# Performance work log

Hardware: AMD Instinct MI355X
Metric: run time of the kernel (lower is better)

## Reference

```python
import jax, jax.numpy as jnp
import numpy as np
from jax import lax

LONG_EDGE = 1024
MAX_SIZE = 1333.0
STRIDES = (4, 8, 16, 32, 64)
SIZES = (32, 64, 128, 256, 512)
RATIOS = (0.5, 1.0, 2.0)
PRE_NMS_TOPK = 6000
POST_NMS_TOPK = 1000
NMS_THRESH = 0.7
NUM_CH = 256


def _gen_anchors_level(scale, ratios, shape, stride):
    # faithful copy of generate_anchors_keras (numpy, static)
    scales, ratios = np.meshgrid(np.array([scale], dtype=np.float64), np.array(ratios, dtype=np.float64))
    scales = scales.flatten(); ratios = ratios.flatten()
    size_ratios = stride * stride / ratios
    widths = np.round(np.sqrt(size_ratios))
    heights = np.round(widths * ratios)
    widths = widths * (scales / stride)
    heights = heights * (scales / stride)
    shifts_y = np.arange(0, shape[0]) * stride + (stride - 1) / 2
    shifts_x = np.arange(0, shape[1]) * stride + (stride - 1) / 2
    shifts_x, shifts_y = np.meshgrid(shifts_x, shifts_y)
    box_widths, box_centers_x = np.meshgrid(widths, shifts_x)
    box_heights, box_centers_y = np.meshgrid(heights, shifts_y)
    box_centers = np.stack([box_centers_y, box_centers_x], axis=2).reshape([-1, 2])
    box_sizes = np.stack([box_heights, box_widths], axis=2).reshape([-1, 2])
    boxes = np.concatenate([box_centers - 0.5 * (box_sizes - 1), box_centers + 0.5 * (box_sizes - 1)], axis=1)
    boxes[:, [2, 3]] += 1
    return boxes[:, [1, 0, 3, 2]].astype(np.float32)


def all_anchors():
    shapes = [(int(np.ceil(LONG_EDGE / s)),) * 2 for s in STRIDES]
    return np.concatenate([_gen_anchors_level(SIZES[i], RATIOS, shapes[i], STRIDES[i]) for i in range(len(STRIDES))], axis=0)


def conv2d(x, w, b, padding):
    y = lax.conv_general_dilated(x, w, (1, 1), padding, dimension_numbers=('NCHW', 'OIHW', 'NCHW'))
    return y + b[None, :, None, None]


def decode_bbox_target(deltas, anchors):
    # deltas, anchors: [K,4]
    txty, twth = deltas[:, :2], deltas[:, 2:]
    x1y1, x2y2 = anchors[:, :2], anchors[:, 2:]
    waha = x2y2 - x1y1
    xaya = (x2y2 + x1y1) * 0.5
    clipv = jnp.float32(np.log(MAX_SIZE / 16.0))
    wbhb = jnp.exp(jnp.minimum(twth, clipv)) * waha
    xbyb = txty * waha + xaya
    return jnp.concatenate([xbyb - wbhb * 0.5, xbyb + wbhb * 0.5], axis=1)


def clip_boxes(b, h, w):
    # faithful to source: x clamped to window[0]=h, y to window[1]=w
    return jnp.stack([b[:, 0].clip(0.0, h), b[:, 1].clip(0.0, w), b[:, 2].clip(0.0, h), b[:, 3].clip(0.0, w)], 1)


def nms_keep(boxes, thresh):
    # boxes sorted by descending score; greedy NMS over full IoU matrix
    x1, y1, x2, y2 = boxes[:, 0], boxes[:, 1], boxes[:, 2], boxes[:, 3]
    areas = (x2 - x1) * (y2 - y1)
    iw = jnp.clip(jnp.minimum(x2[:, None], x2[None, :]) - jnp.maximum(x1[:, None], x1[None, :]), 0.0)
    ih = jnp.clip(jnp.minimum(y2[:, None], y2[None, :]) - jnp.maximum(y1[:, None], y1[None, :]), 0.0)
    inter = iw * ih
    iou = inter / (areas[:, None] + areas[None, :] - inter)
    n = boxes.shape[0]
    sup = iou > thresh
    idxs = jnp.arange(n)
    def body(i, keep):
        row = sup[i] & (idxs > i)
        return jnp.where(keep[i], keep & ~row, keep)
    return lax.fori_loop(0, n, body, jnp.ones((n,), bool))


def rpn_forward(image, feats, w0, b0, wcls, bcls, wbox, bbox):
    labels, boxes_l = [], []
    for f in feats:
        hidden = jax.nn.relu(conv2d(f, w0, b0, 'SAME'))
        cls = conv2d(hidden, wcls, bcls, 'VALID')   # [1,A,H,W]
        box = conv2d(hidden, wbox, bbox, 'VALID')   # [1,4A,H,W]
        labels.append(jnp.transpose(cls, (0, 2, 3, 1)).reshape(1, -1, 1))
        boxes_l.append(jnp.transpose(box, (0, 2, 3, 1)).reshape(1, -1, 4))
    scores = jnp.concatenate(labels, axis=1)[0, :, 0]          # [N]
    box_logits = jnp.concatenate(boxes_l, axis=1)[0]           # [N,4]
    anchors = jnp.asarray(all_anchors())                       # [N,4]
    k = min(PRE_NMS_TOPK, anchors.shape[0])
    _, order = lax.top_k(scores, k)
    deltas = box_logits[order]
    pre_anch = anchors[order]
    dec = decode_bbox_target(deltas, pre_anch)
    h, w = float(image.shape[2]), float(image.shape[3])
    boxes = clip_boxes(dec, h, w)
    keep = nms_keep(lax.stop_gradient(boxes), NMS_THRESH)
    sel = jnp.argsort(~keep)[:POST_NMS_TOPK]  # stable: kept boxes in score order, then pad slots
    proposals = jnp.where(keep[sel][:, None], boxes[sel], 0.0)
    return proposals


def setup_inputs() -> dict:
    key = jax.random.key(0)
    ks = jax.random.split(key, 9)
    hw = [256, 128, 64, 32, 16]
    inp = {'image': jax.random.normal(ks[0], (1, 3, 1024, 1024), jnp.float32)}
    for i, s in enumerate(hw):
        inp[f'feat{i}'] = jax.random.normal(jax.random.fold_in(ks[1], i), (1, NUM_CH, s, s), jnp.float32)
    inp['w0'] = jax.random.normal(ks[2], (NUM_CH, NUM_CH, 3, 3), jnp.float32) * 0.01
    inp['b0'] = jnp.zeros((NUM_CH,), jnp.float32)
    inp['wcls'] = jax.random.normal(ks[3], (3, NUM_CH, 1, 1), jnp.float32) * 0.01
    inp['bcls'] = jnp.zeros((3,), jnp.float32)
    inp['wbox'] = jax.random.normal(ks[4], (12, NUM_CH, 1, 1), jnp.float32) * 0.01
    inp['bbox'] = jnp.zeros((12,), jnp.float32)
    return inp


def reference(image, feat0, feat1, feat2, feat3, feat4, w0, b0, wcls, bcls, wbox, bbox):
    feats = [feat0, feat1, feat2, feat3, feat4]
    return rpn_forward(image, feats, w0, b0, wcls, bcls, wbox, bbox)
```

## Files before the change

### kernel.cpp

```cpp
#include <hip/hip_runtime.h>
#include <cstdint>

typedef unsigned long long u64;
typedef unsigned int u32;
typedef unsigned short ushort;
typedef __attribute__((ext_vector_type(8))) short short8;
typedef __attribute__((ext_vector_type(4))) float f32x4;
typedef __attribute__((ext_vector_type(4))) double f64x4;

#define A_TOTAL 261888
#define NPIX    87296
#define KTOP    6000
#define KTARGET 7800
#define NWORDS  94
#define CANDMAX 8192
#define PIXMAX  8192
#define NBINS   16384

#if defined(__has_builtin)
#if __has_builtin(__builtin_amdgcn_mfma_f64_16x16x4f64)
#define HAVE_DGEMM 1
#endif
#endif
#ifndef HAVE_DGEMM
#define HAVE_DGEMM 0
#endif

__device__ __forceinline__ u64 score_key64(double s) {
  u64 u = (u64)__double_as_longlong(s);
  return (u & 0x8000000000000000ULL) ? ~u : (u | 0x8000000000000000ULL);
}
__device__ __forceinline__ u32 key32(float s) {
  u32 u = __float_as_uint(s);
  return (u & 0x80000000u) ? ~u : (u | 0x80000000u);
}
__device__ __forceinline__ ushort f2bf(float f) {
  u32 u = __float_as_uint(f);
  u32 r = (u + 0x7FFFu + ((u >> 16) & 1u)) >> 16;
  return (ushort)r;
}
__device__ __forceinline__ void pix_level(int pix, int& l, int& off) {
  if (pix < 65536)      { l = 0; off = 0; }
  else if (pix < 81920) { l = 1; off = 65536; }
  else if (pix < 86016) { l = 2; off = 81920; }
  else if (pix < 87040) { l = 3; off = 86016; }
  else                  { l = 4; off = 87040; }
}

__global__ void k_prep_w(const float* __restrict__ w0, double* __restrict__ wt64,
                         ushort* __restrict__ wkf) {
  int i = blockIdx.x * 256 + threadIdx.x;
  if (i < 256 * 2304) {
    int o = i & 255;
    int ictap = i >> 8;
    float v = w0[o * 2304 + ictap];
    wt64[(size_t)ictap * 256 + o] = (double)v;
    int ic = ictap / 9;
    int tap = ictap - ic * 9;
    int w = o >> 6, mt = (o >> 4) & 3, l15 = o & 15;
    int ch = ic >> 5, kk = ic & 31;
    int l4 = kk >> 3, e = kk & 7;
    int lane = l4 * 16 + l15;
    wkf[((((w * 4 + mt) * 8 + ch) * 9 + tap) << 9) + lane * 8 + e] = f2bf(v);
  }
}

__global__ void k_probe(u32* __restrict__ flag) {
#if HAVE_DGEMM
  int l = threadIdx.x;
  int m = l & 15, kq = l >> 4;
  double a = (double)(1 + m * 4 + kq);
  double b = (double)(1 + m * 4 + kq * 67);
  f64x4 c = {0.0, 0.0, 0.0, 0.0};
  c = __builtin_amdgcn_mfma_f64_16x16x4f64(a, b, c, 0, 0, 0);
  bool ok = true;
  #pragma unroll
  for (int r = 0; r < 4; ++r) {
    int row = 4 * kq + r, col = m;
    double e = 0.0;
    for (int k = 0; k < 4; ++k)
      e += (double)(1 + row * 4 + k) * (double)(1 + col * 4 + k * 67);
    if (c[r] != e) ok = false;
  }
  u64 bal = __ballot(ok);
  if (l == 0) *flag = (bal == ~0ULL) ? 1u : 0u;
#else
  if (threadIdx.x == 0) *flag = 0u;
#endif
}

__global__ __launch_bounds__(256, 2) void k_conv_mfma(
    const float* __restrict__ f0, const float* __restrict__ f1,
    const float* __restrict__ f2, const float* __restrict__ f3,
    const float* __restrict__ f4,
    const ushort* __restrict__ wkf, const float* __restrict__ b0,
    const float* __restrict__ wcls, const float* __restrict__ bcls,
    float* __restrict__ scr)
{
  __shared__ ushort xsl[100][40];
  __shared__ float  part[3][64][17];

  int b = blockIdx.x;
  int l, tb;
  if (b < 1024)      { l = 0; tb = b; }
  else if (b < 1280) { l = 1; tb = b - 1024; }
  else if (b < 1344) { l = 2; tb = b - 1280; }
  else if (b < 1360) { l = 3; tb = b - 1344; }
  else               { l = 4; tb = b - 1360; }
  const float* feat = (l == 0) ? f0 : (l == 1) ? f1 : (l == 2) ? f2 : (l == 3) ? f3 : f4;
  int Hh = 256 >> l;
  int HW = Hh * Hh;
  int pixOff = (l == 0) ? 0 : (l == 1) ? 65536 : (l == 2) ? 81920 : (l == 3) ? 86016 : 87040;
  int shl = 5 - l;
  int ty = (tb >> shl) << 3;
  int tx = (tb & ((1 << shl) - 1)) << 3;

  int tid = threadIdx.x;
  int w = tid >> 6;
  int lane = tid & 63;
  int l15 = lane & 15;
  int l4 = lane >> 4;

  f32x4 zz = {0.f, 0.f, 0.f, 0.f};
  f32x4 acc[4][4];
  #pragma unroll
  for (int mt = 0; mt < 4; ++mt)
    #pragma unroll
    for (int tt = 0; tt < 4; ++tt) acc[mt][tt] = zz;

  for (int ch = 0; ch < 8; ++ch) {
    __syncthreads();
    for (int e = tid; e < 3200; e += 256) {
      int icl = e / 100;
      int sp = e - icl * 100;
      int yy = sp / 10;
      int xx = sp - yy * 10;
      int gy = ty + yy - 1, gx = tx + xx - 1;
      float v = 0.f;
      if (gy >= 0 && gy < Hh && gx >= 0 && gx < Hh)
        v = feat[(ch * 32 + icl) * HW + gy * Hh + gx];
      xsl[sp][icl] = f2bf(v);
    }
    __syncthreads();
    #pragma unroll
    for (int tap = 0; tap < 9; ++tap) {
      int dy = tap / 3;
      int dx = tap - dy * 3;
      short8 af[4], bf[4];
      #pragma unroll
      for (int mt = 0; mt < 4; ++mt) {
        int abase = ((((w * 4 + mt) * 8 + ch) * 9 + tap) << 9) + (lane << 3);
        af[mt] = *(const short8*)(wkf + abase);
      }
      #pragma unroll
      for (int tt = 0; tt < 4; ++tt) {
        int p = (tt << 4) + l15;
        int sp = ((p >> 3) + dy) * 10 + (p & 7) + dx;
        bf[tt] = *(const short8*)&xsl[sp][l4 << 3];
      }
      #pragma unroll
      for (int mt = 0; mt < 4; ++mt)
        #pragma unroll
        for (int tt = 0; tt < 4; ++tt)
          acc[mt][tt] = __builtin_amdgcn_mfma_f32_16x16x32_bf16(af[mt], bf[tt], acc[mt][tt], 0, 0, 0);
    }
  }

  float pr[3][4];
  #pragma unroll
  for (int kk = 0; kk < 3; ++kk)
    #pragma unroll
    for (int tt = 0; tt < 4; ++tt) pr[kk][tt] = 0.f;
  #pragma unroll
  for (int mt = 0; mt < 4; ++mt) {
    #pragma unroll
    for (int r = 0; r < 4; ++r) {
      int oc = (w << 6) + (mt << 4) + (l4 << 2) + r;
      float bb = b0[oc];
      float c0 = wcls[oc], c1 = wcls[256 + oc], c2 = wcls[512 + oc];
      #pragma unroll
      for (int tt = 0; tt < 4; ++tt) {
        float v = acc[mt][tt][r] + bb;
        v = v > 0.f ? v : 0.f;
        pr[0][tt] = fmaf(c0, v, pr[0][tt]);
        pr[1][tt] = fmaf(c1, v, pr[1][tt]);
        pr[2][tt] = fmaf(c2, v, pr[2][tt]);
      }
    }
  }
  __syncthreads();
  #pragma unroll
  for (int kk = 0; kk < 3; ++kk)
    #pragma unroll
    for (int tt = 0; tt < 4; ++tt)
      part[kk][(tt << 4) + l15][(w << 2) + l4] = pr[kk][tt];
  __syncthreads();
  if (tid < 192) {
    int kk = tid >> 6;
    int px = tid & 63;
    float s = 0.f;
    #pragma unroll
    for (int q = 0; q < 16; ++q) s += part[kk][px][q];
    int pix = pixOff + (ty + (px >> 3)) * Hh + (tx + (px & 7));
    scr[pix * 3 + kk] = s + bcls[kk];
  }
}

__global__ void k_hist1(const float* __restrict__ scr, u32* __restrict__ bins) {
  __shared__ u32 h[NBINS];
  int tid = threadIdx.x;
  for (int idx = tid; idx < NBINS; idx += 256) h[idx] = 0;
  __syncthreads();
  for (int i = blockIdx.x * 256 + tid; i < A_TOTAL; i += gridDim.x * 256)
    atomicAdd(&h[key32(scr[i]) >> 18], 1u);
  __syncthreads();
  for (int idx = tid; idx < NBINS; idx += 256) {
    u32 v = h[idx];
    if (v) atomicAdd(&bins[idx], v);
  }
}

__global__ void k_scan1(const u32* __restrict__ bins, u32* __restrict__ meta) {
  __shared__ u32 psum[256];
  int tid = threadIdx.x;
  u32 s = 0;
  for (int u = 0; u < 64; ++u) s += bins[tid * 64 + u];
  psum[tid] = s;
  __syncthreads();
  if (tid == 0) {
    u32 run = 0;
    for (int t = 255; t >= 0; --t) { u32 tmp = psum[t]; psum[t] = run; run += tmp; }
  }
  __syncthreads();
  u32 cum = psum[tid];
  if (cum < (u32)KTARGET) {
    for (int u = 63; u >= 0; --u) {
      u32 bv = bins[tid * 64 + u];
      u32 nc = cum + bv;
      if (nc >= (u32)KTARGET) {
        meta[0] = (u32)(tid * 64 + u);
        meta[2] = cum;
        break;
      }
      cum = nc;
    }
  }
}

__global__ void k_hist2(const float* __restrict__ scr, const u32* __restrict__ meta,
                        u32* __restrict__ sub) {
  int i = blockIdx.x * 256 + threadIdx.x;
  if (i < A_TOTAL) {
    u32 k = key32(scr[i]);
    if ((k >> 18) == meta[0]) atomicAdd(&sub[(k >> 10) & 0xFFu], 1u);
  }
}

__global__ void k_scan2(const u32* __restrict__ sub, u32* __restrict__ meta) {
  if (threadIdx.x == 0) {
    u32 b = meta[0];
    u32 c = meta[2];
    u32 T = b << 18;
    for (int u = 255; u >= 0; --u) {
      c += sub[u];
      if (c >= (u32)KTARGET) { T = (b << 18) | ((u32)u << 10); break; }
    }
    meta[3] = (T >= (2u << 10)) ? (T - (2u << 10)) : 0u;
  }
}

__global__ void k_cnt2(const float* __restrict__ scr, const u32* __restrict__ meta,
                       u32* __restrict__ blkCnt, u32* __restrict__ blkCntP) {
  __shared__ u32 wc[4], wcp[4];
  int tid = threadIdx.x;
  int lane = tid & 63, wv = tid >> 6;
  u32 T = meta[3];
  int i = blockIdx.x * 256 + tid;
  bool qa = (i < A_TOTAL) && (key32(scr[i]) >= T);
  u64 ba = __ballot(qa);
  bool qp = false;
  if (i < NPIX)
    qp = (key32(scr[i * 3 + 0]) >= T) || (key32(scr[i * 3 + 1]) >= T) || (key32(scr[i * 3 + 2]) >= T);
  u64 bp = __ballot(qp);
  if (lane == 0) { wc[wv] = (u32)__popcll(ba); wcp[wv] = (u32)__popcll(bp); }
  __syncthreads();
  if (tid == 0) {
    blkCnt[blockIdx.x]  = wc[0] + wc[1] + wc[2] + wc[3];
    blkCntP[blockIdx.x] = wcp[0] + wcp[1] + wcp[2] + wcp[3];
  }
}

__global__ __launch_bounds__(1024) void k_scanblk2(const u32* __restrict__ blkCnt,
                                                   u32* __restrict__ blkOff,
                                                   u32* __restrict__ totA,
                                                   const u32* __restrict__ blkCntP,
                                                   u32* __restrict__ blkOffP,
                                                   u32* __restrict__ totP) {
  __shared__ u32 buf[2][1024];
  int tid = threadIdx.x;
  for (int pass = 0; pass < 2; ++pass) {
    const u32* src_ = pass ? blkCntP : blkCnt;
    u32* dst_ = pass ? blkOffP : blkOff;
    u32* tot_ = pass ? totP : totA;
    u32 v = (tid < 1023) ? src_[tid] : 0u;
    buf[0][tid] = v;
    __syncthreads();
    int src = 0;
    for (int d = 1; d < 1024; d <<= 1) {
      u32 t = buf[src][tid] + ((tid >= d) ? buf[src][tid - d] : 0u);
      buf[src ^ 1][tid] = t;
      src ^= 1;
      __syncthreads();
    }
    if (tid < 1023) dst_[tid] = buf[src][tid] - v;
    if (tid == 0) tot_[0] = buf[src][1022];
    __syncthreads();
  }
}

__global__ void k_fill2(const float* __restrict__ scr, const u32* __restrict__ meta,
                        const u32* __restrict__ blkOff, const u32* __restrict__ blkOffP,
                        u32* __restrict__ candIdx, u32* __restrict__ pixList,
                        u32* __restrict__ pixMap) {
  __shared__ u32 wbase[4], wbaseP[4];
  int tid = threadIdx.x;
  int lane = tid & 63, wv = tid >> 6;
  u32 T = meta[3];
  int i = blockIdx.x * 256 + tid;
  bool qa = (i < A_TOTAL) && (key32(scr[i]) >= T);
  u64 ba = __ballot(qa);
  bool qp = false;
  if (i < NPIX)
    qp = (key32(scr[i * 3 + 0]) >= T) || (key32(scr[i * 3 + 1]) >= T) || (key32(scr[i * 3 + 2]) >= T);
  u64 bp = __ballot(qp);
  if (lane == 0) { wbase[wv] = (u32)__popcll(ba); wbaseP[wv] = (u32)__popcll(bp); }
  __syncthreads();
  if (tid == 0) {
    u32 r = blkOff[blockIdx.x];
    #pragma unroll
    for (int w2 = 0; w2 < 4; ++w2) { u32 t = wbase[w2]; wbase[w2] = r; r += t; }
    u32 rp = blkOffP[blockIdx.x];
    #pragma unroll
    for (int w2 = 0; w2 < 4; ++w2) { u32 t = wbaseP[w2]; wbaseP[w2] = rp; rp += t; }
  }
  __syncthreads();
  if (qa) {
    u32 rank = (u32)__popcll(ba & ((1ULL << lane) - 1ULL));
    u32 pos = wbase[wv] + rank;
    if (pos < CANDMAX) candIdx[pos] = (u32)i;
  }
  if (qp) {
    u32 rank = (u32)__popcll(bp & ((1ULL << lane) - 1ULL));
    u32 pos = wbaseP[wv] + rank;
    if (pos < PIXMAX) { pixList[pos] = (u32)i; pixMap[i] = pos; }
  }
}

#define KCH 288
__global__ __launch_bounds__(256, 3) void k_hidden_mfma(
    const float* __restrict__ f0, const float* __restrict__ f1,
    const float* __restrict__ f2, const float* __restrict__ f3,
    const float* __restrict__ f4,
    const double* __restrict__ wt64, const float* __restrict__ b0,
    const u32* __restrict__ pixList, const u32* __restrict__ meta,
    double* __restrict__ hbuf)
{
#if HAVE_DGEMM
  __shared__ float patch[2][KCH][16];
  __shared__ int sValid[16], sY[16], sX[16], sW[16], sL[16];
  if (meta[8] == 0) return;
  int tid = threadIdx.x;
  int base = blockIdx.x * 16;
  u32 np = meta[4];
  if (np > PIXMAX) np = PIXMAX;
  if (base >= (int)np) return;

  if (tid < 16) {
    int slot = base + tid;
    int v = slot < (int)np;
    sValid[tid] = v;
    int pix = v ? (int)pixList[slot] : 0;
    int l, off;
    pix_level(pix, l, off);
    int W = 256 >> l;
    int idx = pix - off;
    sL[tid] = l;
    sW[tid] = W;
    sY[tid] = idx >> (8 - l);
    sX[tid] = idx & (W - 1);
  }
  __syncthreads();

  auto stage = [&](int cb, int pb) {
    for (int t = tid; t < 1536; t += 256) {
      int s = t & 15;
      int rem = t >> 4;
      int icl = rem / 3;
      int dy = rem - icl * 3;
      int ic = cb * 32 + icl;
      float v0 = 0.f, v1 = 0.f, v2 = 0.f;
      if (sValid[s]) {
        int l = sL[s], W = sW[s], y = sY[s], x = sX[s];
        const float* feat = (l == 0) ? f0 : (l == 1) ? f1 : (l == 2) ? f2 : (l == 3) ? f3 : f4;
        int gy = y + dy - 1;
        if (gy >= 0 && gy < W) {
          const float* rowp = feat + ic * W * W + gy * W;
          if (x - 1 >= 0) v0 = rowp[x - 1];
          v1 = rowp[x];
          if (x + 1 < W) v2 = rowp[x + 1];
        }
      }
      int kb = icl * 9 + dy * 3;
      patch[pb][kb + 0][s] = v0;
      patch[pb][kb + 1][s] = v1;
      patch[pb][kb + 2][s] = v2;
    }
  };

  int lane = tid & 63, w = tid >> 6;
  int m = lane & 15, kq = lane >> 4;
  f64x4 acc[4];
  #pragma unroll
  for (int mt = 0; mt < 4; ++mt) acc[mt] = f64x4{0.0, 0.0, 0.0, 0.0};

  stage(0, 0);
  __syncthreads();
  for (int cb = 0; cb < 8; ++cb) {
    if (cb < 7) stage(cb + 1, (cb + 1) & 1);
    const float (*pc)[16] = patch[cb & 1];
    for (int ks = 0; ks < KCH / 4; ++ks) {
      double bv = (double)pc[ks * 4 + kq][m];
      const double* wr = wt64 + (size_t)(cb * KCH + ks * 4 + kq) * 256 + w * 64 + m;
      #pragma unroll
      for (int mt = 0; mt < 4; ++mt)
        acc[mt] = __builtin_amdgcn_mfma_f64_16x16x4f64(wr[mt * 16], bv, acc[mt], 0, 0, 0);
    }
    __syncthreads();
  }

  int slot = base + m;
  bool pv = sValid[m];
  #pragma unroll
  for (int mt = 0; mt < 4; ++mt) {
    #pragma unroll
    for (int r = 0; r < 4; ++r) {
      int oc = w * 64 + mt * 16 + 4 * kq + r;
      if (pv) {
        double t2 = acc[mt][r] + (double)b0[oc];
        hbuf[(size_t)slot * 256 + oc] = t2 > 0.0 ? t2 : 0.0;
      }
    }
  }
#endif
}

#define KC 576
__global__ __launch_bounds__(256, 4) void k_hidden_valu(
    const float* __restrict__ f0, const float* __restrict__ f1,
    const float* __restrict__ f2, const float* __restrict__ f3,
    const float* __restrict__ f4,
    const double* __restrict__ wt64, const float* __restrict__ b0,
    const u32* __restrict__ pixList, const u32* __restrict__ meta,
    double* __restrict__ hbuf)
{
  __shared__ __align__(16) float patch[2][KC][8];
  __shared__ int sValid[8], sY[8], sX[8], sW[8], sL[8];
  if (meta[8] != 0) return;

  int tid = threadIdx.x;
  int base = blockIdx.x * 8;
  u32 np = meta[4];
  if (np > PIXMAX) np = PIXMAX;
  if (base >= (int)np) return;

  if (tid < 8) {
    int slot = base + tid;
    int v = slot < (int)np;
    sValid[tid] = v;
    int pix = v ? (int)pixList[slot] : 0;
    int l, off;
    pix_level(pix, l, off);
    int W = 256 >> l;
    int idx = pix - off;
    sL[tid] = l;
    sW[tid] = W;
    sY[tid] = idx >> (8 - l);
    sX[tid] = idx & (W - 1);
  }
  __syncthreads();

  auto stage = [&](int c, int pb) {
    for (int t = tid; t < 1536; t += 256) {
      int s = t / 192;
      int rem = t - s * 192;
      int icl = rem / 3;
      int dy = rem - icl * 3;
      int ic = c * 64 + icl;
      float v0 = 0.f, v1 = 0.f, v2 = 0.f;
      if (sValid[s]) {
        int l = sL[s], W = sW[s], y = sY[s], x = sX[s];
        const float* feat = (l == 0) ? f0 : (l == 1) ? f1 : (l == 2) ? f2 : (l == 3) ? f3 : f4;
        int gy = y + dy - 1;
        if (gy >= 0 && gy < W) {
          const float* rowp = feat + ic * W * W + gy * W;
          if (x - 1 >= 0) v0 = rowp[x - 1];
          v1 = rowp[x];
          if (x + 1 < W) v2 = rowp[x + 1];
        }
      }
      int kb = icl * 9 + dy * 3;
      patch[pb][kb + 0][s] = v0;
      patch[pb][kb + 1][s] = v1;
      patch[pb][kb + 2][s] = v2;
    }
  };

  stage(0, 0);
  __syncthreads();

  double h[8];
  #pragma unroll
  for (int s = 0; s < 8; ++s) h[s] = 0.0;

  for (int c = 0; c < 4; ++c) {
    if (c < 3) stage(c + 1, (c + 1) & 1);
    const double* wcol = wt64 + (size_t)(c * KC) * 256 + tid;
    const float (*pc)[8] = patch[c & 1];
    for (int kk = 0; kk < KC; ++kk) {
      double wv_ = wcol[(size_t)kk * 256];
      float4 pa = *(const float4*)&pc[kk][0];
      float4 pb2 = *(const float4*)&pc[kk][4];
      h[0] = fma(wv_, (double)pa.x, h[0]);
      h[1] = fma(wv_, (double)pa.y, h[1]);
      h[2] = fma(wv_, (double)pa.z, h[2]);
      h[3] = fma(wv_, (double)pa.w, h[3]);
      h[4] = fma(wv_, (double)pb2.x, h[4]);
      h[5] = fma(wv_, (double)pb2.y, h[5]);
      h[6] = fma(wv_, (double)pb2.z, h[6]);
      h[7] = fma(wv_, (double)pb2.w, h[7]);
    }
    __syncthreads();
  }

  double bb = (double)b0[tid];
  #pragma unroll
  for (int s = 0; s < 8; ++s) {
    if (sValid[s]) {
      double t = h[s] + bb;
      hbuf[(size_t)(base + s) * 256 + tid] = t > 0.0 ? t : 0.0;
    }
  }
}

__global__ __launch_bounds__(256, 4) void k_heads(
    const float* __restrict__ wcls, const float* __restrict__ bcls,
    const float* __restrict__ wbox, const float* __restrict__ bbox,
    const u32* __restrict__ candIdx, const u32* __restrict__ pixMap,
    const u32* __restrict__ meta, const double* __restrict__ hbuf,
    u64* __restrict__ candKey, u32* __restrict__ candPack, double* __restrict__ candDelta)
{
  __shared__ double wavePart[8][5][4];
  __shared__ int sIdx[8], sValid[8], sR[8], sPS[8];
  int tid = threadIdx.x;
  int lane = tid & 63;
  int wv = tid >> 6;
  int base = blockIdx.x * 8;
  u32 cnt = meta[1];
  if (cnt > CANDMAX) cnt = CANDMAX;

  if (base >= (int)cnt) {
    if (tid < 8) {
      candKey[base + tid] = 0ULL;
      candPack[base + tid] = 0xFFFFFFFFu;
    }
    return;
  }

  if (tid < 8) {
    int slot = base + tid;
    int v = slot < (int)cnt;
    sValid[tid] = v;
    int aidx = v ? (int)candIdx[slot] : 0;
    sIdx[tid] = aidx;
    int pix = aidx / 3;
    sR[tid] = aidx - pix * 3;
    sPS[tid] = v ? (int)pixMap[pix] : 0;
  }
  __syncthreads();

  for (int s = 0; s < 8; ++s) {
    if (!sValid[s]) continue;
    int r = sR[s];
    double hv = hbuf[(size_t)sPS[s] * 256 + tid];
    double p0 = (double)wcls[r * 256 + tid] * hv;
    double p1 = (double)wbox[(r * 4 + 0) * 256 + tid] * hv;
    double p2 = (double)wbox[(r * 4 + 1) * 256 + tid] * hv;
    double p3 = (double)wbox[(r * 4 + 2) * 256 + tid] * hv;
    double p4 = (double)wbox[(r * 4 + 3) * 256 + tid] * hv;
    #pragma unroll
    for (int d = 32; d; d >>= 1) {
      p0 += __shfl_xor(p0, d);
      p1 += __shfl_xor(p1, d);
      p2 += __shfl_xor(p2, d);
      p3 += __shfl_xor(p3, d);
      p4 += __shfl_xor(p4, d);
    }
    if (lane == 0) {
      wavePart[s][0][wv] = p0;
      wavePart[s][1][wv] = p1;
      wavePart[s][2][wv] = p2;
      wavePart[s][3][wv] = p3;
      wavePart[s][4][wv] = p4;
    }
  }
  __syncthreads();
  if (tid < 40) {
    int s = tid / 5;
    int k = tid - s * 5;
    int slot = base + s;
    if (sValid[s]) {
      double v = wavePart[s][k][0] + wavePart[s][k][1] + wavePart[s][k][2] + wavePart[s][k][3];
      int r = sR[s];
      if (k == 0) {
        double sc_ = v + (double)bcls[r];
        candKey[slot] = score_key64(sc_);
        candPack[slot] = ((u32)sIdx[s] << 13) | (u32)slot;
      } else {
        candDelta[(size_t)slot * 4 + (k - 1)] = v + (double)bbox[r * 4 + (k - 1)];
      }
    } else if (k == 0) {
      candKey[slot] = 0ULL;
      candPack[slot] = 0xFFFFFFFFu;
    }
  }
}

__global__ __launch_bounds__(256) void k_rank(const u64* __restrict__ candKey,
                                              const u32* __restrict__ candPack,
                                              u32* __restrict__ order) {
  __shared__ u64 fk[1024];
  __shared__ u32 fp[1024];
  __shared__ u32 rsum[32][8];
  int tid = threadIdx.x;
  int c = tid & 31;
  int g = tid >> 5;
  int ci = blockIdx.x * 32 + c;
  u64 mk = candKey[ci];
  u32 mp = candPack[ci];
  u32 cnt = 0;
  for (int chunk = 0; chunk < 8; ++chunk) {
    __syncthreads();
    for (int e = tid; e < 1024; e += 256) {
      fk[e] = candKey[chunk * 1024 + e];
      fp[e] = candPack[chunk * 1024 + e];
    }
    __syncthreads();
    int j0 = g * 128;
    #pragma unroll 4
    for (int j = j0; j < j0 + 128; ++j) {
      u64 kj = fk[j];
      cnt += (kj > mk || (kj == mk && fp[j] < mp)) ? 1u : 0u;
    }
  }
  rsum[c][g] = cnt;
  __syncthreads();
  if (tid < 32) {
    u32 rank = 0;
    #pragma unroll
    for (int q = 0; q < 8; ++q) rank += rsum[tid][q];
    if (rank < (u32)KTOP) order[rank] = mp;
  }
}

__global__ void k_decode(const u32* __restrict__ order, const double* __restrict__ candDelta,
                         double* __restrict__ boxesD) {
  int i = blockIdx.x * 64 + threadIdx.x;
  if (i >= KTOP) return;
  u32 pack = order[i];
  u32 slot = pack & 0x1FFFu;
  u32 a = pack >> 13;
  int pix = (int)(a / 3u);
  int r = (int)(a - (u32)pix * 3u);
  int l, off;
  pix_level(pix, l, off);
  int W = 256 >> l;
  int idx = pix - off;
  int y = idx >> (8 - l);
  int x = idx & (W - 1);
  int s = 4 << l;
  double ratio = (r == 0) ? 0.5 : (r == 1) ? 1.0 : 2.0;
  double wq = rint(sqrt((double)(s * s) / ratio));
  double hq = rint(wq * ratio);
  double Wa = wq * 8.0, Ha = hq * 8.0;
  double cx = (double)x * (double)s + (double)(s - 1) * 0.5;
  double cy = (double)y * (double)s + (double)(s - 1) * 0.5;
  double ax1 = (double)(float)(cx - 0.5 * (Wa - 1.0));
  double ay1 = (double)(float)(cy - 0.5 * (Ha - 1.0));
  double ax2 = (double)(float)(cx + 0.5 * (Wa - 1.0) + 1.0);
  double ay2 = (double)(float)(cy + 0.5 * (Ha - 1.0) + 1.0);
  double tx = candDelta[(size_t)slot * 4 + 0], tyv = candDelta[(size_t)slot * 4 + 1];
  double tw = candDelta[(size_t)slot * 4 + 2], th  = candDelta[(size_t)slot * 4 + 3];
  double wa = ax2 - ax1, ha = ay2 - ay1;
  double xa = (ax1 + ax2) * 0.5, ya = (ay1 + ay2) * 0.5;
  double clipv = (double)(float)log(1333.0 / 16.0);
  double wb = exp(fmin(tw, clipv)) * wa;
  double hb = exp(fmin(th, clipv)) * ha;
  double xb = tx * wa + xa;
  double yb = tyv * ha + ya;
  double bx1 = xb - 0.5 * wb, by1 = yb - 0.5 * hb;
  double bx2 = xb + 0.5 * wb, by2 = yb + 0.5 * hb;
  bx1 = fmin(fmax(bx1, 0.0), 1024.0);
  by1 = fmin(fmax(by1, 0.0), 1024.0);
  bx2 = fmin(fmax(bx2, 0.0), 1024.0);
  by2 = fmin(fmax(by2, 0.0), 1024.0);
  boxesD[(size_t)i * 4 + 0] = bx1;
  boxesD[(size_t)i * 4 + 1] = by1;
  boxesD[(size_t)i * 4 + 2] = bx2;
  boxesD[(size_t)i * 4 + 3] = by2;
}

__global__ void k_mask(const double* __restrict__ boxesD, u64* __restrict__ maskA) {
  __shared__ double cbx[64][4];
  int lane = threadIdx.x;
  int bc = blockIdx.x, br = blockIdx.y;
  if (bc < br) return;
  int ci = bc * 64 + lane;
  if (ci < KTOP) {
    cbx[lane][0] = boxesD[(size_t)ci * 4 + 0];
    cbx[lane][1] = boxesD[(size_t)ci * 4 + 1];
    cbx[lane][2] = boxesD[(size_t)ci * 4 + 2];
    cbx[lane][3] = boxesD[(size_t)ci * 4 + 3];
  } else {
    cbx[lane][0] = -1e30; cbx[lane][1] = -1e30; cbx[lane][2] = -1e30; cbx[lane][3] = -1e30;
  }
  __syncthreads();
  int ri = br * 64 + lane;
  if (ri >= KTOP) return;
  double rx1 = boxesD[(size_t)ri * 4 + 0], ry1 = boxesD[(size_t)ri * 4 + 1];
  double rx2 = boxesD[(size_t)ri * 4 + 2], ry2 = boxesD[(size_t)ri * 4 + 3];
  double ra = (rx2 - rx1) * (ry2 - ry1);
  u64 bits = 0;
  #pragma unroll 4
  for (int j = 0; j < 64; ++j) {
    int cj = bc * 64 + j;
    double iw = fmin(rx2, cbx[j][2]) - fmax(rx1, cbx[j][0]);
    double ih = fmin(ry2, cbx[j][3]) - fmax(ry1, cbx[j][1]);
    iw = fmax(iw, 0.0); ih = fmax(ih, 0.0);
    double inter = iw * ih;
    double ca = (cbx[j][2] - cbx[j][0]) * (cbx[j][3] - cbx[j][1]);
    double iou = inter / (ra + ca - inter);
    if (cj > ri && iou > 0.7) bits |= (1ULL << j);
  }
  maskA[(size_t)ri * NWORDS + bc] = bits;
}

__global__ __launch_bounds__(1024) void k_nms_reduce(const u64* __restrict__ maskA,
                                                     u32* __restrict__ keep) {
  __shared__ u64 rm[NWORDS];
  int tid = threadIdx.x;
  int wv = tid >> 6, lane = tid & 63;
  for (int i = tid; i < NWORDS; i += 1024) rm[i] = 0ULL;
  __syncthreads();
  u64 diagNext = maskA[(size_t)lane * NWORDS + 0];
  int keptTot = 0;
  for (int c = 0; c < NWORDS; ++c) {
    int rows = KTOP - c * 64; if (rows > 64) rows = 64;
    u64 validM = (rows == 64) ? ~0ULL : ((1ULL << rows) - 1ULL);
    size_t rowbase = (size_t)(c * 64 + lane) * NWORDS;
    bool lv = lane < rows;
    int w0i = c + wv;
    u64 v0 = (lv && w0i      < NWORDS) ? maskA[rowbase + w0i]      : 0ULL;
    u64 v1 = (lv && w0i + 16 < NWORDS) ? maskA[rowbase + w0i + 16] : 0ULL;
    u64 v2 = (lv && w0i + 32 < NWORDS) ? maskA[rowbase + w0i + 32] : 0ULL;
    u64 v3 = (lv && w0i + 48 < NWORDS) ? maskA[rowbase + w0i + 48] : 0ULL;
    u64 v4 = (lv && w0i + 64 < NWORDS) ? maskA[rowbase + w0i + 64] : 0ULL;
    u64 v5 = (lv && w0i + 80 < NWORDS) ? maskA[rowbase + w0i + 80] : 0ULL;
    u64 diag = diagNext;
    if (c + 1 < NWORDS) {
      int nrows = KTOP - (c + 1) * 64; if (nrows > 64) nrows = 64;
      diagNext = (lane < nrows) ? maskA[(size_t)((c + 1) * 64 + lane) * NWORDS + (c + 1)] : 0ULL;
    }
    u64 R = rm[c];
    u64 undec = (~R) & validM;
    u64 km = 0;
    while (undec) {
      int j = __builtin_ctzll(undec);
      km |= (1ULL << j);
      u64 dj = (u64)__shfl((unsigned long long)diag, j);
      undec &= ~(dj | (1ULL << j));
    }
    if (wv == 0 && lane < rows) keep[c * 64 + lane] = (u32)((km >> lane) & 1ULL);
    keptTot += (int)__popcll(km);
    if (keptTot >= 1000) {
      for (int i = (c + 1) * 64 + tid; i < KTOP; i += 1024) keep[i] = 0u;
      return;
    }
    u64 sel = ((km >> lane) & 1ULL) ? ~0ULL : 0ULL;
    v0 &= sel; v1 &= sel; v2 &= sel; v3 &= sel; v4 &= sel; v5 &= sel;
    #pragma unroll
    for (int s = 32; s; s >>= 1) {
      v0 |= (u64)__shfl_xor((unsigned long long)v0, s);
      v1 |= (u64)__shfl_xor((unsigned long long)v1, s);
      v2 |= (u64)__shfl_xor((unsigned long long)v2, s);
      v3 |= (u64)__shfl_xor((unsigned long long)v3, s);
      v4 |= (u64)__shfl_xor((unsigned long long)v4, s);
      v5 |= (u64)__shfl_xor((unsigned long long)v5, s);
    }
    if (lane == 0) {
      if (w0i      < NWORDS) rm[w0i]      |= v0;
      if (w0i + 16 < NWORDS) rm[w0i + 16] |= v1;
      if (w0i + 32 < NWORDS) rm[w0i + 32] |= v2;
      if (w0i + 48 < NWORDS) rm[w0i + 48] |= v3;
      if (w0i + 64 < NWORDS) rm[w0i + 64] |= v4;
      if (w0i + 80 < NWORDS) rm[w0i + 80] |= v5;
    }
    __syncthreads();
  }
}

__global__ __launch_bounds__(1024) void k_emit(const u32* __restrict__ keep,
                                               const double* __restrict__ boxesD,
                                               float* __restrict__ out) {
  __shared__ u32 partial[1024];
  __shared__ u32 excl[1024];
  int tid = threadIdx.x;
  for (int j = tid; j < 4000; j += 1024) out[j] = 0.f;
  int base = tid * 6;
  u32 kv[6];
  u32 c = 0;
  #pragma unroll
  for (int u = 0; u < 6; ++u) {
    int j = base + u;
    kv[u] = (j < KTOP) ? keep[j] : 0u;
    c += kv[u];
  }
  partial[tid] = c;
  __syncthreads();
  if (tid == 0) {
    u32 run = 0;
    for (int t = 0; t < 1024; ++t) { excl[t] = run; run += partial[t]; }
  }
  __syncthreads();
  u32 p = excl[tid];
  #pragma unroll
  for (int u = 0; u < 6; ++u) {
    int j = base + u;
    if (j < KTOP && kv[u]) {
      if (p < 1000u) {
        out[p * 4 + 0] = (float)boxesD[(size_t)j * 4 + 0];
        out[p * 4 + 1] = (float)boxesD[(size_t)j * 4 + 1];
        out[p * 4 + 2] = (float)boxesD[(size_t)j * 4 + 2];
        out[p * 4 + 3] = (float)boxesD[(size_t)j * 4 + 3];
      }
      ++p;
    }
  }
}

extern "C" void kernel_launch(void* const* d_in, const int* in_sizes, int n_in,
                              void* d_out, int out_size, void* d_ws, size_t ws_size,
                              hipStream_t stream) {
  const float* f0   = (const float*)d_in[1];
  const float* f1   = (const float*)d_in[2];
  const float* f2   = (const float*)d_in[3];
  const float* f3   = (const float*)d_in[4];
  const float* f4   = (const float*)d_in[5];
  const float* w0   = (const float*)d_in[6];
  const float* b0   = (const float*)d_in[7];
  const float* wcls = (const float*)d_in[8];
  const float* bcls = (const float*)d_in[9];
  const float* wbox = (const float*)d_in[10];
  const float* bbox = (const float*)d_in[11];
  float* out = (float*)d_out;
  char* ws = (char*)d_ws;

  size_t off = 0;
  auto alloc = [&](size_t bytes) { size_t o = off; off += (bytes + 255) & ~(size_t)255; return o; };
  size_t off_scr  = alloc((size_t)A_TOTAL * 4);
  size_t off_w64  = alloc((size_t)256 * 2304 * 8);
  size_t off_wk   = alloc((size_t)256 * 2304 * 2);
  size_t off_hb   = alloc((size_t)PIXMAX * 256 * 8);
  size_t off_ci   = alloc((size_t)CANDMAX * 4);
  size_t off_ck   = alloc((size_t)CANDMAX * 8);
  size_t off_cp   = alloc((size_t)CANDMAX * 4);
  size_t off_cd   = alloc((size_t)CANDMAX * 4 * 8);
  size_t off_pl   = alloc((size_t)PIXMAX * 4);
  size_t off_pm   = alloc((size_t)NPIX * 4);
  size_t off_box  = alloc((size_t)KTOP * 4 * 8);
  size_t off_ord  = alloc((size_t)KTOP * 4);
  size_t off_keep = alloc((size_t)KTOP * 4);
  size_t off_mask = alloc((size_t)KTOP * NWORDS * 8);
  size_t off_bcnt = alloc((size_t)1024 * 4);
  size_t off_boff = alloc((size_t)1024 * 4);
  size_t off_bcp  = alloc((size_t)1024 * 4);
  size_t off_bop  = alloc((size_t)1024 * 4);
  size_t off_bins = alloc((size_t)NBINS * 4);
  size_t off_sub  = alloc((size_t)256 * 4);
  size_t off_meta = alloc((size_t)64 * 4);
  size_t off_end  = off;
  (void)in_sizes; (void)n_in; (void)out_size; (void)ws_size;

  float*  scr       = (float*)(ws + off_scr);
  double* wt64      = (double*)(ws + off_w64);
  ushort* wkf       = (ushort*)(ws + off_wk);
  double* hbuf      = (double*)(ws + off_hb);
  u32*    candIdx   = (u32*)(ws + off_ci);
  u64*    candKey   = (u64*)(ws + off_ck);
  u32*    candPack  = (u32*)(ws + off_cp);
  double* candDelta = (double*)(ws + off_cd);
  u32*    pixList   = (u32*)(ws + off_pl);
  u32*    pixMap    = (u32*)(ws + off_pm);
  double* boxesD    = (double*)(ws + off_box);
  u32*    order     = (u32*)(ws + off_ord);
  u32*    keep      = (u32*)(ws + off_keep);
  u64*    maskA     = (u64*)(ws + off_mask);
  u32*    blkCnt    = (u32*)(ws + off_bcnt);
  u32*    blkOff    = (u32*)(ws + off_boff);
  u32*    blkCntP   = (u32*)(ws + off_bcp);
  u32*    blkOffP   = (u32*)(ws + off_bop);
  u32*    bins      = (u32*)(ws + off_bins);
  u32*    sub       = (u32*)(ws + off_sub);
  u32*    meta      = (u32*)(ws + off_meta);

  hipMemsetAsync(ws + off_bins, 0, off_end - off_bins, stream);

  k_prep_w<<<2304, 256, 0, stream>>>(w0, wt64, wkf);
  k_probe<<<1, 64, 0, stream>>>(meta + 8);
  k_conv_mfma<<<1364, 256, 0, stream>>>(f0, f1, f2, f3, f4, wkf, b0, wcls, bcls, scr);
  k_hist1<<<64, 256, 0, stream>>>(scr, bins);
  k_scan1<<<1, 256, 0, stream>>>(bins, meta);
  k_hist2<<<1023, 256, 0, stream>>>(scr, meta, sub);
  k_scan2<<<1, 64, 0, stream>>>(sub, meta);
  k_cnt2<<<1023, 256, 0, stream>>>(scr, meta, blkCnt, blkCntP);
  k_scanblk2<<<1, 1024, 0, stream>>>(blkCnt, blkOff, meta + 1, blkCntP, blkOffP, meta + 4);
  k_fill2<<<1023, 256, 0, stream>>>(scr, meta, blkOff, blkOffP, candIdx, pixList, pixMap);
  k_hidden_mfma<<<PIXMAX / 16, 256, 0, stream>>>(f0, f1, f2, f3, f4, wt64, b0, pixList, meta, hbuf);
  k_hidden_valu<<<PIXMAX / 8, 256, 0, stream>>>(f0, f1, f2, f3, f4, wt64, b0, pixList, meta, hbuf);
  k_heads<<<CANDMAX / 8, 256, 0, stream>>>(wcls, bcls, wbox, bbox, candIdx, pixMap, meta, hbuf,
                                           candKey, candPack, candDelta);
  k_rank<<<CANDMAX / 32, 256, 0, stream>>>(candKey, candPack, order);
  k_decode<<<94, 64, 0, stream>>>(order, candDelta, boxesD);
  k_mask<<<dim3(NWORDS, NWORDS), 64, 0, stream>>>(boxesD, maskA);
  k_nms_reduce<<<1, 1024, 0, stream>>>(maskA, keep);
  k_emit<<<1, 1024, 0, stream>>>(keep, boxesD, out);
}
```

Measured before the change: 983.7 us.

## Replace FP64 MFMA hidden-layer path with register-tiled FP64 VALU kernel

Removes the runtime DGEMM probe kernel and the dual MFMA/VALU hidden-layer kernels, replacing them with a single kernel. Each thread computes a 4x4 block of output channels by pixels in FP64 FMAs, reading four weights and a float4 of patch values per k-step. On MI355X, where FP64 MFMA is available, this moves the recomputation of hidden activations from matrix cores to vector ALUs. It saves one launch and the probe, but may be slower if FP64 matrix throughput exceeds VALU throughput on this part.

```diff
diff --git a/kernel.cpp b/kernel.cpp
--- a/kernel.cpp
+++ b/kernel.cpp
@@ -6,7 +6,6 @@
 typedef unsigned short ushort;
 typedef __attribute__((ext_vector_type(8))) short short8;
 typedef __attribute__((ext_vector_type(4))) float f32x4;
-typedef __attribute__((ext_vector_type(4))) double f64x4;
 
 #define A_TOTAL 261888
 #define NPIX    87296
@@ -16,15 +15,6 @@
 #define CANDMAX 8192
 #define PIXMAX  8192
 #define NBINS   16384
-
-#if defined(__has_builtin)
-#if __has_builtin(__builtin_amdgcn_mfma_f64_16x16x4f64)
-#define HAVE_DGEMM 1
-#endif
-#endif
-#ifndef HAVE_DGEMM
-#define HAVE_DGEMM 0
-#endif
 
 __device__ __forceinline__ u64 score_key64(double s) {
   u64 u = (u64)__double_as_longlong(s);
@@ -63,30 +53,6 @@
     int lane = l4 * 16 + l15;
     wkf[((((w * 4 + mt) * 8 + ch) * 9 + tap) << 9) + lane * 8 + e] = f2bf(v);
   }
-}
-
-__global__ void k_probe(u32* __restrict__ flag) {
-#if HAVE_DGEMM
-  int l = threadIdx.x;
-  int m = l & 15, kq = l >> 4;
-  double a = (double)(1 + m * 4 + kq);
-  double b = (double)(1 + m * 4 + kq * 67);
-  f64x4 c = {0.0, 0.0, 0.0, 0.0};
-  c = __builtin_amdgcn_mfma_f64_16x16x4f64(a, b, c, 0, 0, 0);
-  bool ok = true;
-  #pragma unroll
-  for (int r = 0; r < 4; ++r) {
-    int row = 4 * kq + r, col = m;
-    double e = 0.0;
-    for (int k = 0; k < 4; ++k)
-      e += (double)(1 + row * 4 + k) * (double)(1 + col * 4 + k * 67);
-    if (c[r] != e) ok = false;
-  }
-  u64 bal = __ballot(ok);
-  if (l == 0) *flag = (bal == ~0ULL) ? 1u : 0u;
-#else
-  if (threadIdx.x == 0) *flag = 0u;
-#endif
 }
 
 __global__ __launch_bounds__(256, 2) void k_conv_mfma(
@@ -357,7 +323,7 @@
 }
 
 #define KCH 288
-__global__ __launch_bounds__(256, 3) void k_hidden_mfma(
+__global__ __launch_bounds__(256, 4) void k_hidden(
     const float* __restrict__ f0, const float* __restrict__ f1,
     const float* __restrict__ f2, const float* __restrict__ f3,
     const float* __restrict__ f4,
@@ -365,10 +331,9 @@
     const u32* __restrict__ pixList, const u32* __restrict__ meta,
     double* __restrict__ hbuf)
 {
-#if HAVE_DGEMM
   __shared__ float patch[2][KCH][16];
   __shared__ int sValid[16], sY[16], sX[16], sW[16], sL[16];
-  if (meta[8] == 0) return;
+
   int tid = threadIdx.x;
   int base = blockIdx.x * 16;
   u32 np = meta[4];
@@ -417,137 +382,61 @@
     }
   };
 
-  int lane = tid & 63, w = tid >> 6;
-  int m = lane & 15, kq = lane >> 4;
-  f64x4 acc[4];
+  int ocq = tid & 63;
+  int pxq = tid >> 6;
+
+  double acc[4][4];
   #pragma unroll
-  for (int mt = 0; mt < 4; ++mt) acc[mt] = f64x4{0.0, 0.0, 0.0, 0.0};
+  for (int i = 0; i < 4; ++i)
+    #pragma unroll
+    for (int j = 0; j < 4; ++j) acc[i][j] = 0.0;
 
   stage(0, 0);
   __syncthreads();
+
   for (int cb = 0; cb < 8; ++cb) {
     if (cb < 7) stage(cb + 1, (cb + 1) & 1);
     const float (*pc)[16] = patch[cb & 1];
-    for (int ks = 0; ks < KCH / 4; ++ks) {
-      double bv = (double)pc[ks * 4 + kq][m];
-      const double* wr = wt64 + (size_t)(cb * KCH + ks * 4 + kq) * 256 + w * 64 + m;
-      #pragma unroll
-      for (int mt = 0; mt < 4; ++mt)
-        acc[mt] = __builtin_amdgcn_mfma_f64_16x16x4f64(wr[mt * 16], bv, acc[mt], 0, 0, 0);
+    const double* wb_ = wt64 + (size_t)(cb * KCH) * 256 + (ocq << 2);
+    for (int kk = 0; kk < KCH; ++kk) {
+      float4 p4 = *(const float4*)&pc[kk][pxq << 2];
+      double pd0 = (double)p4.x, pd1 = (double)p4.y;
+      double pd2 = (double)p4.z, pd3 = (double)p4.w;
+      const double* wr = wb_ + (size_t)kk * 256;
+      double w0_ = wr[0], w1_ = wr[1], w2_ = wr[2], w3_ = wr[3];
+      acc[0][0] = fma(w0_, pd0, acc[0][0]);
+      acc[0][1] = fma(w0_, pd1, acc[0][1]);
+      acc[0][2] = fma(w0_, pd2, acc[0][2]);
+      acc[0][3] = fma(w0_, pd3, acc[0][3]);
+      acc[1][0] = fma(w1_, pd0, acc[1][0]);
+      acc[1][1] = fma(w1_, pd1, acc[1][1]);
+      acc[1][2] = fma(w1_, pd2, acc[1][2]);
+      acc[1][3] = fma(w1_, pd3, acc[1][3]);
+      acc[2][0] = fma(w2_, pd0, acc[2][0]);
+      acc[2][1] = fma(w2_, pd1, acc[2][1]);
+      acc[2][2] = fma(w2_, pd2, acc[2][2]);
+      acc[2][3] = fma(w2_, pd3, acc[2][3]);
+      acc[3][0] = fma(w3_, pd0, acc[3][0]);
+      acc[3][1] = fma(w3_, pd1, acc[3][1]);
+      acc[3][2] = fma(w3_, pd2, acc[3][2]);
+      acc[3][3] = fma(w3_, pd3, acc[3][3]);
     }
     __syncthreads();
   }
 
-  int slot = base + m;
-  bool pv = sValid[m];
+  double bb0 = (double)b0[(ocq << 2) + 0];
+  double bb1 = (double)b0[(ocq << 2) + 1];
+  double bb2 = (double)b0[(ocq << 2) + 2];
+  double bb3 = (double)b0[(ocq << 2) + 3];
   #pragma unroll
-  for (int mt = 0; mt < 4; ++mt) {
-    #pragma unroll
-    for (int r = 0; r < 4; ++r) {
-      int oc = w * 64 + mt * 16 + 4 * kq + r;
-      if (pv) {
-        double t2 = acc[mt][r] + (double)b0[oc];
-        hbuf[(size_t)slot * 256 + oc] = t2 > 0.0 ? t2 : 0.0;
-      }
-    }
-  }
-#endif
-}
-
-#define KC 576
-__global__ __launch_bounds__(256, 4) void k_hidden_valu(
-    const float* __restrict__ f0, const float* __restrict__ f1,
-    const float* __restrict__ f2, const float* __restrict__ f3,
-    const float* __restrict__ f4,
-    const double* __restrict__ wt64, const float* __restrict__ b0,
-    const u32* __restrict__ pixList, const u32* __restrict__ meta,
-    double* __restrict__ hbuf)
-{
-  __shared__ __align__(16) float patch[2][KC][8];
-  __shared__ int sValid[8], sY[8], sX[8], sW[8], sL[8];
-  if (meta[8] != 0) return;
-
-  int tid = threadIdx.x;
-  int base = blockIdx.x * 8;
-  u32 np = meta[4];
-  if (np > PIXMAX) np = PIXMAX;
-  if (base >= (int)np) return;
-
-  if (tid < 8) {
-    int slot = base + tid;
-    int v = slot < (int)np;
-    sValid[tid] = v;
-    int pix = v ? (int)pixList[slot] : 0;
-    int l, off;
-    pix_level(pix, l, off);
-    int W = 256 >> l;
-    int idx = pix - off;
-    sL[tid] = l;
-    sW[tid] = W;
-    sY[tid] = idx >> (8 - l);
-    sX[tid] = idx & (W - 1);
-  }
-  __syncthreads();
-
-  auto stage = [&](int c, int pb) {
-    for (int t = tid; t < 1536; t += 256) {
-      int s = t / 192;
-      int rem = t - s * 192;
-      int icl = rem / 3;
-      int dy = rem - icl * 3;
-      int ic = c * 64 + icl;
-      float v0 = 0.f, v1 = 0.f, v2 = 0.f;
-      if (sValid[s]) {
-        int l = sL[s], W = sW[s], y = sY[s], x = sX[s];
-        const float* feat = (l == 0) ? f0 : (l == 1) ? f1 : (l == 2) ? f2 : (l == 3) ? f3 : f4;
-        int gy = y + dy - 1;
-        if (gy >= 0 && gy < W) {
-          const float* rowp = feat + ic * W * W + gy * W;
-          if (x - 1 >= 0) v0 = rowp[x - 1];
-          v1 = rowp[x];
-          if (x + 1 < W) v2 = rowp[x + 1];
-        }
-      }
-      int kb = icl * 9 + dy * 3;
-      patch[pb][kb + 0][s] = v0;
-      patch[pb][kb + 1][s] = v1;
-      patch[pb][kb + 2][s] = v2;
-    }
-  };
-
-  stage(0, 0);
-  __syncthreads();
-
-  double h[8];
-  #pragma unroll
-  for (int s = 0; s < 8; ++s) h[s] = 0.0;
-
-  for (int c = 0; c < 4; ++c) {
-    if (c < 3) stage(c + 1, (c + 1) & 1);
-    const double* wcol = wt64 + (size_t)(c * KC) * 256 + tid;
-    const float (*pc)[8] = patch[c & 1];
-    for (int kk = 0; kk < KC; ++kk) {
-      double wv_ = wcol[(size_t)kk * 256];
-      float4 pa = *(const float4*)&pc[kk][0];
-      float4 pb2 = *(const float4*)&pc[kk][4];
-      h[0] = fma(wv_, (double)pa.x, h[0]);
-      h[1] = fma(wv_, (double)pa.y, h[1]);
-      h[2] = fma(wv_, (double)pa.z, h[2]);
-      h[3] = fma(wv_, (double)pa.w, h[3]);
-      h[4] = fma(wv_, (double)pb2.x, h[4]);
-      h[5] = fma(wv_, (double)pb2.y, h[5]);
-      h[6] = fma(wv_, (double)pb2.z, h[6]);
-      h[7] = fma(wv_, (double)pb2.w, h[7]);
-    }
-    __syncthreads();
-  }
-
-  double bb = (double)b0[tid];
-  #pragma unroll
-  for (int s = 0; s < 8; ++s) {
+  for (int j = 0; j < 4; ++j) {
+    int s = (pxq << 2) + j;
     if (sValid[s]) {
-      double t = h[s] + bb;
-      hbuf[(size_t)(base + s) * 256 + tid] = t > 0.0 ? t : 0.0;
+      double* dst = &hbuf[(size_t)(base + s) * 256 + (ocq << 2)];
+      double o0 = acc[0][j] + bb0; dst[0] = o0 > 0.0 ? o0 : 0.0;
+      double o1 = acc[1][j] + bb1; dst[1] = o1 > 0.0 ? o1 : 0.0;
+      double o2 = acc[2][j] + bb2; dst[2] = o2 > 0.0 ? o2 : 0.0;
+      double o3 = acc[3][j] + bb3; dst[3] = o3 > 0.0 ? o3 : 0.0;
     }
   }
 }
@@ -925,7 +814,6 @@
   hipMemsetAsync(ws + off_bins, 0, off_end - off_bins, stream);
 
   k_prep_w<<<2304, 256, 0, stream>>>(w0, wt64, wkf);
-  k_probe<<<1, 64, 0, stream>>>(meta + 8);
   k_conv_mfma<<<1364, 256, 0, stream>>>(f0, f1, f2, f3, f4, wkf, b0, wcls, bcls, scr);
   k_hist1<<<64, 256, 0, stream>>>(scr, bins);
   k_scan1<<<1, 256, 0, stream>>>(bins, meta);
@@ -934,8 +822,7 @@
   k_cnt2<<<1023, 256, 0, stream>>>(scr, meta, blkCnt, blkCntP);
   k_scanblk2<<<1, 1024, 0, stream>>>(blkCnt, blkOff, meta + 1, blkCntP, blkOffP, meta + 4);
   k_fill2<<<1023, 256, 0, stream>>>(scr, meta, blkOff, blkOffP, candIdx, pixList, pixMap);
-  k_hidden_mfma<<<PIXMAX / 16, 256, 0, stream>>>(f0, f1, f2, f3, f4, wt64, b0, pixList, meta, hbuf);
-  k_hidden_valu<<<PIXMAX / 8, 256, 0, stream>>>(f0, f1, f2, f3, f4, wt64, b0, pixList, meta, hbuf);
+  k_hidden<<<PIXMAX / 16, 256, 0, stream>>>(f0, f1, f2, f3, f4, wt64, b0, pixList, meta, hbuf);
   k_heads<<<CANDMAX / 8, 256, 0, stream>>>(wcls, bcls, wbox, bbox, candIdx, pixMap, meta, hbuf,
                                            candKey, candPack, candDelta);
   k_rank<<<CANDMAX / 32, 256, 0, stream>>>(candKey, candPack, order);
```

New measurement: 894.3 us. -9.1%, faster.
